# Performance work log

Measured on AMD Instinct MI355X. Metric: run time of the kernel, lower is better.

## Reference

```python
import jax, jax.numpy as jnp
import numpy as np

N_NODES = 50000
N_EDGES = 800000
IN_CH, HID_CH, OUT_CH = 128, 128, 64


def setup_inputs() -> dict:
    key = jax.random.key(0)
    k1, k2, k3, k4, k5, k6 = jax.random.split(key, 6)
    x = jax.random.normal(k1, (N_NODES, IN_CH), dtype=jnp.float32)
    edge_index = jax.random.randint(k2, (2, N_EDGES), 0, N_NODES, dtype=jnp.int64)
    # nn.Linear params: W [out, in], b [out]
    W1 = jax.random.normal(k3, (HID_CH, IN_CH), dtype=jnp.float32) / np.sqrt(IN_CH)
    b1 = jax.random.normal(k4, (HID_CH,), dtype=jnp.float32) * 0.01
    W2 = jax.random.normal(k5, (OUT_CH, HID_CH), dtype=jnp.float32) / np.sqrt(HID_CH)
    b2 = jax.random.normal(k6, (OUT_CH,), dtype=jnp.float32) * 0.01
    return {"x": x, "edge_index": edge_index, "W1": W1, "b1": b1, "W2": W2, "b2": b2}


def _aggregate(x, edge_index):
    # Faithful to SimpleGNN.aggregate: deg from ROW counts, normalization gathered at DST (col).
    row, col = edge_index[0], edge_index[1]
    n = x.shape[0]
    deg = jnp.bincount(row, length=n).astype(x.dtype)
    deg_inv = jnp.where(deg > 0, 1.0 / deg, 0.0)
    # out[dst] += x[src] * deg_inv[dst]  ==  segment_sum(x[src] by dst) * deg_inv[dst]
    agg = jax.ops.segment_sum(x[row], col, num_segments=n)
    return agg * deg_inv[:, None]


def reference(x, edge_index, W1, b1, W2, b2):
    h = x @ W1.T + b1                 # [N, hidden]
    h = _aggregate(h, edge_index)     # degree-normalized scatter-add
    out = h @ W2.T + b2               # [N, out]
    return out
```

## Files before the change

### kernel.cpp

```cpp
#include <hip/hip_runtime.h>
#include <hip/hip_bf16.h>


#define IN_CH   128
#define OUT_CH  64
#define NCHUNK  64
#define NRANGE  8
#define RBINS   6272
#define NRANGE_H 4
#define RBINS_H 12544
#define MC_BLOCKS 33
#define MC_PAD  40
#define YROWS   32
#define PLACE_BLOCKS (NCHUNK * NRANGE)
#define SMEM_FLOATS (IN_CH * OUT_CH + YROWS * (IN_CH + 4))

typedef unsigned short u16;
typedef unsigned int u32;

static __device__ inline float bfu32_lo(u32 u) { return __uint_as_float(u << 16); }
static __device__ inline float bfu32_hi(u32 u) { return __uint_as_float(u & 0xffff0000u); }
static __device__ inline u16 f2bf(float f) {
    __hip_bfloat16 h = __float2bfloat16(f);
    return *reinterpret_cast<u16*>(&h);
}

static __device__ inline int detect_stride_wave(const int* __restrict__ ei) {
    int lane = threadIdx.x & 63;
    int idx = (lane < 32) ? (2 * lane + 1) : 1;
    int v = ei[idx];
    unsigned long long m = __ballot((v != 0) && (lane < 32));
    return (m == 0ull) ? 2 : 1;
}

__global__ __launch_bounds__(256) void mk_prep(const float* __restrict__ W1,
                                               const float* __restrict__ b1,
                                               const float* __restrict__ W2,
                                               const int* __restrict__ ei,
                                               float* __restrict__ M,
                                               float* __restrict__ c,
                                               u16* __restrict__ row_slab,
                                               u16* __restrict__ col_slab,
                                               int n_edges, int n_nodes) {
    __shared__ u32 bins[RBINS_H];
    int b = blockIdx.x;
    int tid = threadIdx.x;
    if (b < MC_PAD) {
        int t = b * 256 + tid;
        if (t < IN_CH * OUT_CH) {
            int o = t & (OUT_CH - 1);
            int i = t >> 6;
            float acc = 0.f;
            for (int h = 0; h < 128; ++h)
                acc += W1[h * 128 + i] * W2[o * 128 + h];
            M[i * OUT_CH + o] = acc;
        } else if (t < IN_CH * OUT_CH + OUT_CH) {
            int o = t - IN_CH * OUT_CH;
            float acc = 0.f;
            for (int h = 0; h < 128; ++h)
                acc += b1[h] * W2[o * 128 + h];
            c[o] = acc;
        }
        return;
    }
    int hb = b - MC_PAD;
    int range = hb & (NRANGE_H - 1);
    int chunk = hb >> 2;

    int range_size = (n_nodes + NRANGE_H - 1) / NRANGE_H;
    int lo = range * range_size;
    int hi = lo + range_size; if (hi > n_nodes) hi = n_nodes;
    int nbins = hi - lo;
    if (nbins <= 0) return;

    int stride = detect_stride_wave(ei);
    for (int i = tid; i < nbins; i += 256) bins[i] = 0u;
    __syncthreads();

    size_t e0 = (size_t)chunk * n_edges / NCHUNK;
    size_t e1 = (size_t)(chunk + 1) * n_edges / NCHUNK;
    size_t cnt = e1 - e0;
    const int* rp = ei;
    const int* cp = ei + (size_t)n_edges * stride;

    size_t i = tid;
    int s[8], d[8];
    for (; i + 1792 < cnt; i += 2048) {
#pragma unroll
        for (int k = 0; k < 8; ++k) s[k] = rp[(e0 + i + 256 * k) * stride];
#pragma unroll
        for (int k = 0; k < 8; ++k) d[k] = cp[(e0 + i + 256 * k) * stride];
#pragma unroll
        for (int k = 0; k < 8; ++k) {
            if (s[k] >= lo && s[k] < hi) atomicAdd(&bins[s[k] - lo], 1u);
            if (d[k] >= lo && d[k] < hi && (unsigned)s[k] < (unsigned)n_nodes)
                atomicAdd(&bins[d[k] - lo], 0x10000u);
        }
    }
    for (; i < cnt; i += 256) {
        int ss = rp[(e0 + i) * stride];
        int dd = cp[(e0 + i) * stride];
        if (ss >= lo && ss < hi) atomicAdd(&bins[ss - lo], 1u);
        if (dd >= lo && dd < hi && (unsigned)ss < (unsigned)n_nodes)
            atomicAdd(&bins[dd - lo], 0x10000u);
    }
    __syncthreads();

    size_t base = (size_t)chunk * n_nodes + lo;
    for (int k = tid; k < nbins; k += 256) {
        u32 v = bins[k];
        row_slab[base + k] = (u16)(v & 0xFFFFu);
        col_slab[base + k] = (u16)(v >> 16);
    }
}

__global__ __launch_bounds__(256) void mk_choff(u16* __restrict__ row_slab,
                                                u16* __restrict__ col_slab,
                                                int* __restrict__ deg_row,
                                                int* __restrict__ cnt_col,
                                                int* __restrict__ cursor_part,
                                                int* __restrict__ bsums,
                                                int n_nodes) {
    __shared__ int sm[256];
    int t = threadIdx.x;
    int n = blockIdx.x * 256 + t;
    int run = 0;
    if (n < n_nodes) {
        int sum = 0;
#pragma unroll 8
        for (int ch = 0; ch < NCHUNK; ++ch)
            sum += row_slab[(size_t)ch * n_nodes + n];
        deg_row[n] = sum;
#pragma unroll 8
        for (int ch = 0; ch < NCHUNK; ++ch) {
            int v = col_slab[(size_t)ch * n_nodes + n];
            col_slab[(size_t)ch * n_nodes + n] = (u16)run;
            run += v;
        }
        cnt_col[n] = run;
    }
    sm[t] = run;
    __syncthreads();
    for (int d = 1; d < 256; d <<= 1) {
        int add = (t >= d) ? sm[t - d] : 0;
        __syncthreads();
        sm[t] += add;
        __syncthreads();
    }
    if (n < n_nodes) cursor_part[n] = sm[t] - run;
    if (t == 255) bsums[blockIdx.x] = sm[t];
}

static __device__ void block_bscan(const int* __restrict__ bsums, int nb,
                                   int* __restrict__ bscan) {
    int t = threadIdx.x;
    int v = (t < nb) ? bsums[t] : 0;
    bscan[t] = v;
    __syncthreads();
    for (int d = 1; d < 256; d <<= 1) {
        int add = (t >= d) ? bscan[t - d] : 0;
        __syncthreads();
        bscan[t] += add;
        __syncthreads();
    }
    bscan[t] -= v;
    __syncthreads();
}

__global__ __launch_bounds__(256) void mk_place_y(const int* __restrict__ ei,
                                                  const int* __restrict__ cursor_part,
                                                  const int* __restrict__ bsums,
                                                  const u16* __restrict__ col_slab,
                                                  int* __restrict__ csr_src,
                                                  const float* __restrict__ x,
                                                  const float* __restrict__ M,
                                                  u16* __restrict__ y,
                                                  int n_edges, int n_nodes, int nb) {
    __shared__ float smem[SMEM_FLOATS];
    int b = blockIdx.x;
    int tid = threadIdx.x;

    if (b < PLACE_BLOCKS) {
        int* rank = (int*)smem;
        int* bscan = (int*)smem + RBINS;
        block_bscan(bsums, nb, bscan);

        int range = b & (NRANGE - 1);
        int chunk = b >> 3;
        int range_size = (n_nodes + NRANGE - 1) / NRANGE;
        int lo = range * range_size;
        int hi = lo + range_size; if (hi > n_nodes) hi = n_nodes;
        if (hi <= lo) return;

        int stride = detect_stride_wave(ei);
        for (int i = tid; i < hi - lo; i += 256) rank[i] = 0;
        __syncthreads();

        size_t e0 = (size_t)chunk * n_edges / NCHUNK;
        size_t e1 = (size_t)(chunk + 1) * n_edges / NCHUNK;
        size_t cnt = e1 - e0;
        const int* rp = ei;
        const int* cp = ei + (size_t)n_edges * stride;
        size_t slab_base = (size_t)chunk * n_nodes;

        size_t i = tid;
        int s[8], d[8], cpart[8], coff[8];
        for (; i + 1792 < cnt; i += 2048) {
#pragma unroll
            for (int k = 0; k < 8; ++k) s[k] = rp[(e0 + i + 256 * k) * stride];
#pragma unroll
            for (int k = 0; k < 8; ++k) d[k] = cp[(e0 + i + 256 * k) * stride];
#pragma unroll
            for (int k = 0; k < 8; ++k) {
                int dc = (d[k] >= lo && d[k] < hi) ? d[k] : lo;
                cpart[k] = cursor_part[dc];
                coff[k]  = (int)col_slab[slab_base + dc];
            }
#pragma unroll
            for (int k = 0; k < 8; ++k) {
                if (d[k] >= lo && d[k] < hi && (unsigned)s[k] < (unsigned)n_nodes) {
                    int r = atomicAdd(&rank[d[k] - lo], 1);
                    csr_src[cpart[k] + bscan[d[k] >> 8] + coff[k] + r] = s[k];
                }
            }
        }
        for (; i < cnt; i += 256) {
            int ss = rp[(e0 + i) * stride];
            int dd = cp[(e0 + i) * stride];
            if (dd >= lo && dd < hi && (unsigned)ss < (unsigned)n_nodes) {
                int r = atomicAdd(&rank[dd - lo], 1);
                csr_src[cursor_part[dd] + bscan[dd >> 8] + (int)col_slab[slab_base + dd] + r] = ss;
            }
        }
        return;
    }

    int t = b - PLACE_BLOCKS;
    float* Ms = smem;
    float (*xs)[IN_CH + 4] = (float(*)[IN_CH + 4])(smem + IN_CH * OUT_CH);
    int tx = tid & 15;
    int ty = tid >> 4;
    int row0 = t * YROWS;
    if (row0 >= n_nodes) return;

    const float4* Mv = (const float4*)M;
    float4* Msv = (float4*)Ms;
#pragma unroll
    for (int k = 0; k < 8; ++k) Msv[tid + 256 * k] = Mv[tid + 256 * k];

    for (int f = tid; f < YROWS * 32; f += 256) {
        int r = f >> 5, kq = f & 31;
        float4 v = make_float4(0.f, 0.f, 0.f, 0.f);
        if (row0 + r < n_nodes)
            v = *(const float4*)&x[(size_t)(row0 + r) * IN_CH + 4 * kq];
        *(float4*)&xs[r][4 * kq] = v;
    }
    __syncthreads();

    float4 acc0 = make_float4(0.f, 0.f, 0.f, 0.f);
    float4 acc1 = make_float4(0.f, 0.f, 0.f, 0.f);

    for (int k = 0; k < IN_CH; k += 4) {
        float4 xr0 = *(const float4*)&xs[ty][k];
        float4 xr1 = *(const float4*)&xs[ty + 16][k];
        float4 m0 = *(const float4*)&Ms[(k + 0) * OUT_CH + 4 * tx];
        float4 m1 = *(const float4*)&Ms[(k + 1) * OUT_CH + 4 * tx];
        float4 m2 = *(const float4*)&Ms[(k + 2) * OUT_CH + 4 * tx];
        float4 m3 = *(const float4*)&Ms[(k + 3) * OUT_CH + 4 * tx];
        acc0.x = fmaf(xr0.x, m0.x, acc0.x); acc0.y = fmaf(xr0.x, m0.y, acc0.y);
        acc0.z = fmaf(xr0.x, m0.z, acc0.z); acc0.w = fmaf(xr0.x, m0.w, acc0.w);
        acc0.x = fmaf(xr0.y, m1.x, acc0.x); acc0.y = fmaf(xr0.y, m1.y, acc0.y);
        acc0.z = fmaf(xr0.y, m1.z, acc0.z); acc0.w = fmaf(xr0.y, m1.w, acc0.w);
        acc0.x = fmaf(xr0.z, m2.x, acc0.x); acc0.y = fmaf(xr0.z, m2.y, acc0.y);
        acc0.z = fmaf(xr0.z, m2.z, acc0.z); acc0.w = fmaf(xr0.z, m2.w, acc0.w);
        acc0.x = fmaf(xr0.w, m3.x, acc0.x); acc0.y = fmaf(xr0.w, m3.y, acc0.y);
        acc0.z = fmaf(xr0.w, m3.z, acc0.z); acc0.w = fmaf(xr0.w, m3.w, acc0.w);
        acc1.x = fmaf(xr1.x, m0.x, acc1.x); acc1.y = fmaf(xr1.x, m0.y, acc1.y);
        acc1.z = fmaf(xr1.x, m0.z, acc1.z); acc1.w = fmaf(xr1.x, m0.w, acc1.w);
        acc1.x = fmaf(xr1.y, m1.x, acc1.x); acc1.y = fmaf(xr1.y, m1.y, acc1.y);
        acc1.z = fmaf(xr1.y, m1.z, acc1.z); acc1.w = fmaf(xr1.y, m1.w, acc1.w);
        acc1.x = fmaf(xr1.z, m2.x, acc1.x); acc1.y = fmaf(xr1.z, m2.y, acc1.y);
        acc1.z = fmaf(xr1.z, m2.z, acc1.z); acc1.w = fmaf(xr1.z, m2.w, acc1.w);
        acc1.x = fmaf(xr1.w, m3.x, acc1.x); acc1.y = fmaf(xr1.w, m3.y, acc1.y);
        acc1.z = fmaf(xr1.w, m3.z, acc1.z); acc1.w = fmaf(xr1.w, m3.w, acc1.w);
    }

    int r0 = row0 + ty;
    int r1 = row0 + ty + 16;
    if (r0 < n_nodes) {
        ushort4 s4;
        s4.x = f2bf(acc0.x); s4.y = f2bf(acc0.y);
        s4.z = f2bf(acc0.z); s4.w = f2bf(acc0.w);
        *(ushort4*)&y[(size_t)r0 * OUT_CH + 4 * tx] = s4;
    }
    if (r1 < n_nodes) {
        ushort4 s4;
        s4.x = f2bf(acc1.x); s4.y = f2bf(acc1.y);
        s4.z = f2bf(acc1.z); s4.w = f2bf(acc1.w);
        *(ushort4*)&y[(size_t)r1 * OUT_CH + 4 * tx] = s4;
    }
}

__global__ __launch_bounds__(256) void mk_agg_final(const int* __restrict__ cursor_part,
                                                    const int* __restrict__ bsums,
                                                    const int* __restrict__ cnt_col,
                                                    const int* __restrict__ csr_src,
                                                    const int* __restrict__ deg_row,
                                                    const uint2* __restrict__ yv,
                                                    const float* __restrict__ c,
                                                    const float* __restrict__ b2,
                                                    float* __restrict__ out,
                                                    int n_nodes, int nb) {
    __shared__ int bscan[256];
    block_bscan(bsums, nb, bscan);

    int wave = threadIdx.x >> 6;
    int lane = threadIdx.x & 63;
    int dsub = lane >> 4;
    int ch   = lane & 15;
    int d = blockIdx.x * 16 + wave * 4 + dsub;
    if (d >= n_nodes) return;

    int start = cursor_part[d] + bscan[d >> 8];
    int cnt = cnt_col[d];
    int end = start + cnt;
    int e1m = end - 1;
    float a0 = 0.f, a1 = 0.f, a2 = 0.f, a3 = 0.f;
    for (int j = start; j < end; j += 8) {
        int idx[8], srcs[8];
#pragma unroll
        for (int k = 0; k < 8; ++k) {
            int t = j + k;
            idx[k] = t > e1m ? e1m : t;
        }
#pragma unroll
        for (int k = 0; k < 8; ++k) srcs[k] = csr_src[idx[k]];
        uint2 u[8];
#pragma unroll
        for (int k = 0; k < 8; ++k) u[k] = yv[(size_t)srcs[k] * 16 + ch];
#pragma unroll
        for (int k = 1; k < 8; ++k)
            if (j + k >= end) { u[k].x = 0u; u[k].y = 0u; }
#pragma unroll
        for (int k = 0; k < 8; ++k) {
            a0 += bfu32_lo(u[k].x);
            a1 += bfu32_hi(u[k].x);
            a2 += bfu32_lo(u[k].y);
            a3 += bfu32_hi(u[k].y);
        }
    }
    int dr = deg_row[d];
    float di = (dr > 0) ? (1.0f / (float)dr) : 0.f;
    float fc = di * (float)cnt;
    float4 cv = ((const float4*)c)[ch];
    float4 bv = ((const float4*)b2)[ch];
    float4 o;
    o.x = di * a0 + fc * cv.x + bv.x;
    o.y = di * a1 + fc * cv.y + bv.y;
    o.z = di * a2 + fc * cv.z + bv.z;
    o.w = di * a3 + fc * cv.w + bv.w;
    ((float4*)(out + (size_t)d * OUT_CH))[ch] = o;
}

extern "C" void kernel_launch(void* const* d_in, const int* in_sizes, int n_in,
                              void* d_out, int out_size, void* d_ws, size_t ws_size,
                              hipStream_t stream) {
    const float* x  = (const float*)d_in[0];
    const int*   ei = (const int*)d_in[1];
    const float* W1 = (const float*)d_in[2];
    const float* b1 = (const float*)d_in[3];
    const float* W2 = (const float*)d_in[4];
    const float* b2 = (const float*)d_in[5];
    float* out = (float*)d_out;

    const int n_nodes = in_sizes[0] / IN_CH;
    const int n_edges = in_sizes[1] / 2;

    const size_t slab_bytes = (((size_t)NCHUNK * n_nodes * 2) + 127) & ~(size_t)127;
    const size_t csr_bytes  = ((size_t)n_edges * 4 + 127) & ~(size_t)127;

    char* ws = (char*)d_ws;
    float* M        = (float*)(ws);
    float* c        = (float*)(ws + 32768);
    int*   deg_row  = (int*)  (ws + 33152);
    int*   cnt_col  = (int*)  (ws + 233216);
    int*   cursor   = (int*)  (ws + 433280);
    int*   bsums    = (int*)  (ws + 633344);
    u16*   row_slab = (u16*)  (ws + 637440);
    u16*   col_slab = (u16*)  (ws + 637440 + slab_bytes);
    int*   csr_src  = (int*)  (ws + 637440 + 2 * slab_bytes);
    u16*   y        = (u16*)  (ws + 637440 + 2 * slab_bytes + csr_bytes);

    const int y_blocks = (n_nodes + YROWS - 1) / YROWS;
    const int nb = (n_nodes + 255) / 256;

    mk_prep<<<MC_PAD + NCHUNK * NRANGE_H, 256, 0, stream>>>(
        W1, b1, W2, ei, M, c, row_slab, col_slab, n_edges, n_nodes);

    mk_choff<<<nb, 256, 0, stream>>>(row_slab, col_slab, deg_row, cnt_col,
                                     cursor, bsums, n_nodes);

    mk_place_y<<<PLACE_BLOCKS + y_blocks, 256, 0, stream>>>(
        ei, cursor, bsums, col_slab, csr_src, x, M, y, n_edges, n_nodes, nb);

    mk_agg_final<<<(n_nodes + 15) / 16, 256, 0, stream>>>(
        cursor, bsums, cnt_col, csr_src, deg_row, (const uint2*)y, c, b2, out,
        n_nodes, nb);
}
```

Measured before the change: 154.2 us.

## Move block-sum scan into choff via last-block counter and split y GEMM across launches

```diff
diff --git a/kernel.cpp b/kernel.cpp
--- a/kernel.cpp
+++ b/kernel.cpp
@@ -9,7 +9,6 @@
 #define RBINS   6272
 #define NRANGE_H 4
 #define RBINS_H 12544
-#define MC_BLOCKS 33
 #define MC_PAD  40
 #define YROWS   32
 #define PLACE_BLOCKS (NCHUNK * NRANGE)
@@ -33,209 +32,11 @@
     return (m == 0ull) ? 2 : 1;
 }
 
-__global__ __launch_bounds__(256) void mk_prep(const float* __restrict__ W1,
-                                               const float* __restrict__ b1,
-                                               const float* __restrict__ W2,
-                                               const int* __restrict__ ei,
-                                               float* __restrict__ M,
-                                               float* __restrict__ c,
-                                               u16* __restrict__ row_slab,
-                                               u16* __restrict__ col_slab,
-                                               int n_edges, int n_nodes) {
-    __shared__ u32 bins[RBINS_H];
-    int b = blockIdx.x;
+static __device__ inline void y_unit(int t, const float* __restrict__ x,
+                                     const float* __restrict__ M,
+                                     u16* __restrict__ y, float* smem,
+                                     int n_nodes) {
     int tid = threadIdx.x;
-    if (b < MC_PAD) {
-        int t = b * 256 + tid;
-        if (t < IN_CH * OUT_CH) {
-            int o = t & (OUT_CH - 1);
-            int i = t >> 6;
-            float acc = 0.f;
-            for (int h = 0; h < 128; ++h)
-                acc += W1[h * 128 + i] * W2[o * 128 + h];
-            M[i * OUT_CH + o] = acc;
-        } else if (t < IN_CH * OUT_CH + OUT_CH) {
-            int o = t - IN_CH * OUT_CH;
-            float acc = 0.f;
-            for (int h = 0; h < 128; ++h)
-                acc += b1[h] * W2[o * 128 + h];
-            c[o] = acc;
-        }
-        return;
-    }
-    int hb = b - MC_PAD;
-    int range = hb & (NRANGE_H - 1);
-    int chunk = hb >> 2;
-
-    int range_size = (n_nodes + NRANGE_H - 1) / NRANGE_H;
-    int lo = range * range_size;
-    int hi = lo + range_size; if (hi > n_nodes) hi = n_nodes;
-    int nbins = hi - lo;
-    if (nbins <= 0) return;
-
-    int stride = detect_stride_wave(ei);
-    for (int i = tid; i < nbins; i += 256) bins[i] = 0u;
-    __syncthreads();
-
-    size_t e0 = (size_t)chunk * n_edges / NCHUNK;
-    size_t e1 = (size_t)(chunk + 1) * n_edges / NCHUNK;
-    size_t cnt = e1 - e0;
-    const int* rp = ei;
-    const int* cp = ei + (size_t)n_edges * stride;
-
-    size_t i = tid;
-    int s[8], d[8];
-    for (; i + 1792 < cnt; i += 2048) {
-#pragma unroll
-        for (int k = 0; k < 8; ++k) s[k] = rp[(e0 + i + 256 * k) * stride];
-#pragma unroll
-        for (int k = 0; k < 8; ++k) d[k] = cp[(e0 + i + 256 * k) * stride];
-#pragma unroll
-        for (int k = 0; k < 8; ++k) {
-            if (s[k] >= lo && s[k] < hi) atomicAdd(&bins[s[k] - lo], 1u);
-            if (d[k] >= lo && d[k] < hi && (unsigned)s[k] < (unsigned)n_nodes)
-                atomicAdd(&bins[d[k] - lo], 0x10000u);
-        }
-    }
-    for (; i < cnt; i += 256) {
-        int ss = rp[(e0 + i) * stride];
-        int dd = cp[(e0 + i) * stride];
-        if (ss >= lo && ss < hi) atomicAdd(&bins[ss - lo], 1u);
-        if (dd >= lo && dd < hi && (unsigned)ss < (unsigned)n_nodes)
-            atomicAdd(&bins[dd - lo], 0x10000u);
-    }
-    __syncthreads();
-
-    size_t base = (size_t)chunk * n_nodes + lo;
-    for (int k = tid; k < nbins; k += 256) {
-        u32 v = bins[k];
-        row_slab[base + k] = (u16)(v & 0xFFFFu);
-        col_slab[base + k] = (u16)(v >> 16);
-    }
-}
-
-__global__ __launch_bounds__(256) void mk_choff(u16* __restrict__ row_slab,
-                                                u16* __restrict__ col_slab,
-                                                int* __restrict__ deg_row,
-                                                int* __restrict__ cnt_col,
-                                                int* __restrict__ cursor_part,
-                                                int* __restrict__ bsums,
-                                                int n_nodes) {
-    __shared__ int sm[256];
-    int t = threadIdx.x;
-    int n = blockIdx.x * 256 + t;
-    int run = 0;
-    if (n < n_nodes) {
-        int sum = 0;
-#pragma unroll 8
-        for (int ch = 0; ch < NCHUNK; ++ch)
-            sum += row_slab[(size_t)ch * n_nodes + n];
-        deg_row[n] = sum;
-#pragma unroll 8
-        for (int ch = 0; ch < NCHUNK; ++ch) {
-            int v = col_slab[(size_t)ch * n_nodes + n];
-            col_slab[(size_t)ch * n_nodes + n] = (u16)run;
-            run += v;
-        }
-        cnt_col[n] = run;
-    }
-    sm[t] = run;
-    __syncthreads();
-    for (int d = 1; d < 256; d <<= 1) {
-        int add = (t >= d) ? sm[t - d] : 0;
-        __syncthreads();
-        sm[t] += add;
-        __syncthreads();
-    }
-    if (n < n_nodes) cursor_part[n] = sm[t] - run;
-    if (t == 255) bsums[blockIdx.x] = sm[t];
-}
-
-static __device__ void block_bscan(const int* __restrict__ bsums, int nb,
-                                   int* __restrict__ bscan) {
-    int t = threadIdx.x;
-    int v = (t < nb) ? bsums[t] : 0;
-    bscan[t] = v;
-    __syncthreads();
-    for (int d = 1; d < 256; d <<= 1) {
-        int add = (t >= d) ? bscan[t - d] : 0;
-        __syncthreads();
-        bscan[t] += add;
-        __syncthreads();
-    }
-    bscan[t] -= v;
-    __syncthreads();
-}
-
-__global__ __launch_bounds__(256) void mk_place_y(const int* __restrict__ ei,
-                                                  const int* __restrict__ cursor_part,
-                                                  const int* __restrict__ bsums,
-                                                  const u16* __restrict__ col_slab,
-                                                  int* __restrict__ csr_src,
-                                                  const float* __restrict__ x,
-                                                  const float* __restrict__ M,
-                                                  u16* __restrict__ y,
-                                                  int n_edges, int n_nodes, int nb) {
-    __shared__ float smem[SMEM_FLOATS];
-    int b = blockIdx.x;
-    int tid = threadIdx.x;
-
-    if (b < PLACE_BLOCKS) {
-        int* rank = (int*)smem;
-        int* bscan = (int*)smem + RBINS;
-        block_bscan(bsums, nb, bscan);
-
-        int range = b & (NRANGE - 1);
-        int chunk = b >> 3;
-        int range_size = (n_nodes + NRANGE - 1) / NRANGE;
-        int lo = range * range_size;
-        int hi = lo + range_size; if (hi > n_nodes) hi = n_nodes;
-        if (hi <= lo) return;
-
-        int stride = detect_stride_wave(ei);
-        for (int i = tid; i < hi - lo; i += 256) rank[i] = 0;
-        __syncthreads();
-
-        size_t e0 = (size_t)chunk * n_edges / NCHUNK;
-        size_t e1 = (size_t)(chunk + 1) * n_edges / NCHUNK;
-        size_t cnt = e1 - e0;
-        const int* rp = ei;
-        const int* cp = ei + (size_t)n_edges * stride;
-        size_t slab_base = (size_t)chunk * n_nodes;
-
-        size_t i = tid;
-        int s[8], d[8], cpart[8], coff[8];
-        for (; i + 1792 < cnt; i += 2048) {
-#pragma unroll
-            for (int k = 0; k < 8; ++k) s[k] = rp[(e0 + i + 256 * k) * stride];
-#pragma unroll
-            for (int k = 0; k < 8; ++k) d[k] = cp[(e0 + i + 256 * k) * stride];
-#pragma unroll
-            for (int k = 0; k < 8; ++k) {
-                int dc = (d[k] >= lo && d[k] < hi) ? d[k] : lo;
-                cpart[k] = cursor_part[dc];
-                coff[k]  = (int)col_slab[slab_base + dc];
-            }
-#pragma unroll
-            for (int k = 0; k < 8; ++k) {
-                if (d[k] >= lo && d[k] < hi && (unsigned)s[k] < (unsigned)n_nodes) {
-                    int r = atomicAdd(&rank[d[k] - lo], 1);
-                    csr_src[cpart[k] + bscan[d[k] >> 8] + coff[k] + r] = s[k];
-                }
-            }
-        }
-        for (; i < cnt; i += 256) {
-            int ss = rp[(e0 + i) * stride];
-            int dd = cp[(e0 + i) * stride];
-            if (dd >= lo && dd < hi && (unsigned)ss < (unsigned)n_nodes) {
-                int r = atomicAdd(&rank[dd - lo], 1);
-                csr_src[cursor_part[dd] + bscan[dd >> 8] + (int)col_slab[slab_base + dd] + r] = ss;
-            }
-        }
-        return;
-    }
-
-    int t = b - PLACE_BLOCKS;
     float* Ms = smem;
     float (*xs)[IN_CH + 4] = (float(*)[IN_CH + 4])(smem + IN_CH * OUT_CH);
     int tx = tid & 15;
@@ -301,8 +102,234 @@
     }
 }
 
+__global__ __launch_bounds__(256) void mk_prep(const float* __restrict__ W1,
+                                               const float* __restrict__ b1,
+                                               const float* __restrict__ W2,
+                                               const int* __restrict__ ei,
+                                               float* __restrict__ M,
+                                               float* __restrict__ c,
+                                               u16* __restrict__ row_slab,
+                                               u16* __restrict__ col_slab,
+                                               int* __restrict__ counter,
+                                               int n_edges, int n_nodes) {
+    __shared__ u32 bins[RBINS_H];
+    int b = blockIdx.x;
+    int tid = threadIdx.x;
+    if (b < MC_PAD) {
+        if (b == 0 && tid == 0) *counter = 0;
+        int t = b * 256 + tid;
+        if (t < IN_CH * OUT_CH) {
+            int o = t & (OUT_CH - 1);
+            int i = t >> 6;
+            float acc = 0.f;
+            for (int h = 0; h < 128; ++h)
+                acc += W1[h * 128 + i] * W2[o * 128 + h];
+            M[i * OUT_CH + o] = acc;
+        } else if (t < IN_CH * OUT_CH + OUT_CH) {
+            int o = t - IN_CH * OUT_CH;
+            float acc = 0.f;
+            for (int h = 0; h < 128; ++h)
+                acc += b1[h] * W2[o * 128 + h];
+            c[o] = acc;
+        }
+        return;
+    }
+    int hb = b - MC_PAD;
+    int range = hb & (NRANGE_H - 1);
+    int chunk = hb >> 2;
+
+    int range_size = (n_nodes + NRANGE_H - 1) / NRANGE_H;
+    int lo = range * range_size;
+    int hi = lo + range_size; if (hi > n_nodes) hi = n_nodes;
+    int nbins = hi - lo;
+    if (nbins <= 0) return;
+
+    int stride = detect_stride_wave(ei);
+    for (int i = tid; i < nbins; i += 256) bins[i] = 0u;
+    __syncthreads();
+
+    size_t e0 = (size_t)chunk * n_edges / NCHUNK;
+    size_t e1 = (size_t)(chunk + 1) * n_edges / NCHUNK;
+    size_t cnt = e1 - e0;
+    const int* rp = ei;
+    const int* cp = ei + (size_t)n_edges * stride;
+
+    size_t i = tid;
+    int s[8], d[8];
+    for (; i + 1792 < cnt; i += 2048) {
+#pragma unroll
+        for (int k = 0; k < 8; ++k) s[k] = rp[(e0 + i + 256 * k) * stride];
+#pragma unroll
+        for (int k = 0; k < 8; ++k) d[k] = cp[(e0 + i + 256 * k) * stride];
+#pragma unroll
+        for (int k = 0; k < 8; ++k) {
+            if (s[k] >= lo && s[k] < hi) atomicAdd(&bins[s[k] - lo], 1u);
+            if (d[k] >= lo && d[k] < hi && (unsigned)s[k] < (unsigned)n_nodes)
+                atomicAdd(&bins[d[k] - lo], 0x10000u);
+        }
+    }
+    for (; i < cnt; i += 256) {
+        int ss = rp[(e0 + i) * stride];
+        int dd = cp[(e0 + i) * stride];
+        if (ss >= lo && ss < hi) atomicAdd(&bins[ss - lo], 1u);
+        if (dd >= lo && dd < hi && (unsigned)ss < (unsigned)n_nodes)
+            atomicAdd(&bins[dd - lo], 0x10000u);
+    }
+    __syncthreads();
+
+    size_t base = (size_t)chunk * n_nodes + lo;
+    for (int k = tid; k < nbins; k += 256) {
+        u32 v = bins[k];
+        row_slab[base + k] = (u16)(v & 0xFFFFu);
+        col_slab[base + k] = (u16)(v >> 16);
+    }
+}
+
+__global__ __launch_bounds__(256) void mk_choff_y(u16* __restrict__ row_slab,
+                                                  u16* __restrict__ col_slab,
+                                                  int* __restrict__ deg_row,
+                                                  int* __restrict__ cnt_col,
+                                                  int* __restrict__ cursor_part,
+                                                  int* __restrict__ bsums,
+                                                  int* __restrict__ counter,
+                                                  int* __restrict__ bscan_g,
+                                                  const float* __restrict__ x,
+                                                  const float* __restrict__ M,
+                                                  u16* __restrict__ y,
+                                                  int n_nodes, int nb) {
+    __shared__ float smem[SMEM_FLOATS];
+    __shared__ int islast;
+    int b = blockIdx.x;
+    int t = threadIdx.x;
+
+    if (b >= nb) {
+        y_unit(b - nb, x, M, y, smem, n_nodes);
+        return;
+    }
+
+    int* sm = (int*)smem;
+    int n = b * 256 + t;
+    int run = 0;
+    if (n < n_nodes) {
+        int sum = 0;
+#pragma unroll 8
+        for (int ch = 0; ch < NCHUNK; ++ch)
+            sum += row_slab[(size_t)ch * n_nodes + n];
+        deg_row[n] = sum;
+#pragma unroll 8
+        for (int ch = 0; ch < NCHUNK; ++ch) {
+            int v = col_slab[(size_t)ch * n_nodes + n];
+            col_slab[(size_t)ch * n_nodes + n] = (u16)run;
+            run += v;
+        }
+        cnt_col[n] = run;
+    }
+    sm[t] = run;
+    __syncthreads();
+    for (int d = 1; d < 256; d <<= 1) {
+        int add = (t >= d) ? sm[t - d] : 0;
+        __syncthreads();
+        sm[t] += add;
+        __syncthreads();
+    }
+    if (n < n_nodes) cursor_part[n] = sm[t] - run;
+    if (t == 255) bsums[b] = sm[t];
+
+    __syncthreads();
+    if (t == 0) {
+        __threadfence();
+        int old = atomicAdd(counter, 1);
+        islast = (old == nb - 1);
+    }
+    __syncthreads();
+    if (islast) {
+        int v = (t < nb) ? atomicAdd(&bsums[t], 0) : 0;
+        sm[t] = v;
+        __syncthreads();
+        for (int d = 1; d < 256; d <<= 1) {
+            int add = (t >= d) ? sm[t - d] : 0;
+            __syncthreads();
+            sm[t] += add;
+            __syncthreads();
+        }
+        bscan_g[t] = sm[t] - v;
+    }
+}
+
+__global__ __launch_bounds__(256) void mk_place_y(const int* __restrict__ ei,
+                                                  const int* __restrict__ cursor_part,
+                                                  const int* __restrict__ bscan_g,
+                                                  const u16* __restrict__ col_slab,
+                                                  int* __restrict__ csr_src,
+                                                  const float* __restrict__ x,
+                                                  const float* __restrict__ M,
+                                                  u16* __restrict__ y,
+                                                  int n_edges, int n_nodes,
+                                                  int y_split) {
+    __shared__ float smem[SMEM_FLOATS];
+    int b = blockIdx.x;
+    int tid = threadIdx.x;
+
+    if (b < PLACE_BLOCKS) {
+        int* rank = (int*)smem;
+        int* bscanL = (int*)smem + RBINS;
+
+        int range = b & (NRANGE - 1);
+        int chunk = b >> 3;
+        int range_size = (n_nodes + NRANGE - 1) / NRANGE;
+        int lo = range * range_size;
+        int hi = lo + range_size; if (hi > n_nodes) hi = n_nodes;
+        if (hi <= lo) return;
+
+        int stride = detect_stride_wave(ei);
+        bscanL[tid] = bscan_g[tid];
+        for (int i = tid; i < hi - lo; i += 256) rank[i] = 0;
+        __syncthreads();
+
+        size_t e0 = (size_t)chunk * n_edges / NCHUNK;
+        size_t e1 = (size_t)(chunk + 1) * n_edges / NCHUNK;
+        size_t cnt = e1 - e0;
+        const int* rp = ei;
+        const int* cp = ei + (size_t)n_edges * stride;
+        size_t slab_base = (size_t)chunk * n_nodes;
+
+        size_t i = tid;
+        int s[8], d[8], cpart[8], coff[8];
+        for (; i + 1792 < cnt; i += 2048) {
+#pragma unroll
+            for (int k = 0; k < 8; ++k) s[k] = rp[(e0 + i + 256 * k) * stride];
+#pragma unroll
+            for (int k = 0; k < 8; ++k) d[k] = cp[(e0 + i + 256 * k) * stride];
+#pragma unroll
+            for (int k = 0; k < 8; ++k) {
+                int dc = (d[k] >= lo && d[k] < hi) ? d[k] : lo;
+                cpart[k] = cursor_part[dc];
+                coff[k]  = (int)col_slab[slab_base + dc];
+            }
+#pragma unroll
+            for (int k = 0; k < 8; ++k) {
+                if (d[k] >= lo && d[k] < hi && (unsigned)s[k] < (unsigned)n_nodes) {
+                    int r = atomicAdd(&rank[d[k] - lo], 1);
+                    csr_src[cpart[k] + bscanL[d[k] >> 8] + coff[k] + r] = s[k];
+                }
+            }
+        }
+        for (; i < cnt; i += 256) {
+            int ss = rp[(e0 + i) * stride];
+            int dd = cp[(e0 + i) * stride];
+            if (dd >= lo && dd < hi && (unsigned)ss < (unsigned)n_nodes) {
+                int r = atomicAdd(&rank[dd - lo], 1);
+                csr_src[cursor_part[dd] + bscanL[dd >> 8] + (int)col_slab[slab_base + dd] + r] = ss;
+            }
+        }
+        return;
+    }
+
+    y_unit(y_split + (b - PLACE_BLOCKS), x, M, y, smem, n_nodes);
+}
+
 __global__ __launch_bounds__(256) void mk_agg_final(const int* __restrict__ cursor_part,
-                                                    const int* __restrict__ bsums,
+                                                    const int* __restrict__ bscan_g,
                                                     const int* __restrict__ cnt_col,
                                                     const int* __restrict__ csr_src,
                                                     const int* __restrict__ deg_row,
@@ -310,10 +337,7 @@
                                                     const float* __restrict__ c,
                                                     const float* __restrict__ b2,
                                                     float* __restrict__ out,
-                                                    int n_nodes, int nb) {
-    __shared__ int bscan[256];
-    block_bscan(bsums, nb, bscan);
-
+                                                    int n_nodes) {
     int wave = threadIdx.x >> 6;
     int lane = threadIdx.x & 63;
     int dsub = lane >> 4;
@@ -321,7 +345,7 @@
     int d = blockIdx.x * 16 + wave * 4 + dsub;
     if (d >= n_nodes) return;
 
-    int start = cursor_part[d] + bscan[d >> 8];
+    int start = cursor_part[d] + bscan_g[d >> 8];
     int cnt = cnt_col[d];
     int end = start + cnt;
     int e1m = end - 1;
@@ -386,24 +410,30 @@
     int*   cnt_col  = (int*)  (ws + 233216);
     int*   cursor   = (int*)  (ws + 433280);
     int*   bsums    = (int*)  (ws + 633344);
-    u16*   row_slab = (u16*)  (ws + 637440);
-    u16*   col_slab = (u16*)  (ws + 637440 + slab_bytes);
-    int*   csr_src  = (int*)  (ws + 637440 + 2 * slab_bytes);
-    u16*   y        = (u16*)  (ws + 637440 + 2 * slab_bytes + csr_bytes);
-
-    const int y_blocks = (n_nodes + YROWS - 1) / YROWS;
+    int*   bscan_g  = (int*)  (ws + 634368);
+    int*   counter  = (int*)  (ws + 635392);
+    u16*   row_slab = (u16*)  (ws + 635520);
+    u16*   col_slab = (u16*)  (ws + 635520 + slab_bytes);
+    int*   csr_src  = (int*)  (ws + 635520 + 2 * slab_bytes);
+    u16*   y        = (u16*)  (ws + 635520 + 2 * slab_bytes + csr_bytes);
+
+    const int y_total = (n_nodes + YROWS - 1) / YROWS;
     const int nb = (n_nodes + 255) / 256;
+    int y_split = 512 - nb;
+    if (y_split > y_total) y_split = y_total;
 
     mk_prep<<<MC_PAD + NCHUNK * NRANGE_H, 256, 0, stream>>>(
-        W1, b1, W2, ei, M, c, row_slab, col_slab, n_edges, n_nodes);
-
-    mk_choff<<<nb, 256, 0, stream>>>(row_slab, col_slab, deg_row, cnt_col,
-                                     cursor, bsums, n_nodes);
-
-    mk_place_y<<<PLACE_BLOCKS + y_blocks, 256, 0, stream>>>(
-        ei, cursor, bsums, col_slab, csr_src, x, M, y, n_edges, n_nodes, nb);
+        W1, b1, W2, ei, M, c, row_slab, col_slab, counter, n_edges, n_nodes);
+
+    mk_choff_y<<<nb + y_split, 256, 0, stream>>>(
+        row_slab, col_slab, deg_row, cnt_col, cursor, bsums, counter, bscan_g,
+        x, M, y, n_nodes, nb);
+
+    mk_place_y<<<PLACE_BLOCKS + (y_total - y_split), 256, 0, stream>>>(
+        ei, cursor, bscan_g, col_slab, csr_src, x, M, y, n_edges, n_nodes,
+        y_split);
 
     mk_agg_final<<<(n_nodes + 15) / 16, 256, 0, stream>>>(
-        cursor, bsums, cnt_col, csr_src, deg_row, (const uint2*)y, c, b2, out,
-        n_nodes, nb);
-}
+        cursor, bscan_g, cnt_col, csr_src, deg_row, (const uint2*)y, c, b2, out,
+        n_nodes);
+}
```

After: 156.1 us. No clear change (+1.3%).
